# Kernel tuning notes

Hardware: AMD Instinct MI355X
Metric: run time of the kernel (lower is better)

Reference implementation:

```python
import jax, jax.numpy as jnp
import numpy as np
from jax import lax

N, CIN, FMAPS, H, W, K, LATENT = 8, 512, 512, 64, 64, 3, 512
LRMUL = 1.0
# StyleGAN2 wscale: he_std = gain/sqrt(fan_in); runtime_coef = he_std*lrmul; init_std = 1/lrmul = 1
COEF_W = 1.0 / np.sqrt(K * K * CIN)   # fan_in of conv weight
COEF_S = 1.0 / np.sqrt(LATENT)        # fan_in of modulation dense


def setup_inputs() -> dict:
    key = jax.random.key(0)
    k1, k2, k3, k4, k5 = jax.random.split(key, 5)
    return {
        "x": jax.random.normal(k1, (N, CIN, H, W), jnp.float32),
        "dlatent_vect": jax.random.normal(k2, (N, LATENT), jnp.float32),
        "weight": jax.random.normal(k3, (K, K, CIN, FMAPS), jnp.float32),
        "mod_weight": jax.random.normal(k4, (LATENT, CIN), jnp.float32),
        "mod_bias": jax.random.normal(k5, (CIN,), jnp.float32),
    }


def reference(x, dlatent_vect, weight, mod_weight, mod_bias):
    n = x.shape[0]
    w = weight * COEF_W                                   # [K,K,CIN,FMAPS]
    # style: s = dlatent @ (mod_weight*coef) + bias*lrmul + 1
    s = dlatent_vect @ (mod_weight * COEF_S) + mod_bias * LRMUL + 1.0  # [N,CIN]
    # modulate per-sample weights
    ww = w[None] * s[:, None, None, :, None]              # [N,K,K,CIN,FMAPS]
    # demodulate
    d = lax.rsqrt(jnp.sum(jnp.square(ww), axis=(1, 2, 3)) + 1e-8)  # [N,FMAPS]
    ww = ww * d[:, None, None, None, :]
    # fused modconv: batch-as-groups grouped conv
    x_g = x.reshape(1, n * CIN, H, W)
    w_g = jnp.transpose(ww, (1, 2, 3, 0, 4)).reshape(K, K, CIN, n * FMAPS)
    out = lax.conv_general_dilated(
        x_g, w_g,
        window_strides=(1, 1), padding="SAME",
        dimension_numbers=("NCHW", "HWIO", "NCHW"),
        feature_group_count=n,
    )  # [1, N*FMAPS, H, W]
    return out.reshape(n, FMAPS, H, W)
```

## Files before the change

kernel.cpp:

```cpp
#include <hip/hip_runtime.h>
#include <stdint.h>

typedef unsigned short u16;
typedef __bf16 bf16x8 __attribute__((ext_vector_type(8)));
typedef float  f32x16 __attribute__((ext_vector_type(16)));
typedef short  short8v __attribute__((ext_vector_type(8)));

#define COEF_S 0.044194173824159216f
#define COEF_W 0.014731391274719738f

static __device__ __forceinline__ bf16x8 as_b(short8v v) {
  union { short8v s; bf16x8 b; } u; u.s = v; return u.b;
}

__global__ void style_k(const float* __restrict__ dl, const float* __restrict__ mw,
                        const float* __restrict__ mb, float* __restrict__ s) {
  int idx = blockIdx.x * 256 + threadIdx.x;
  int n = idx >> 9, c = idx & 511;
  const float* dln = dl + n * 512;
  float acc = 0.f;
  for (int l = 0; l < 512; ++l) acc = fmaf(dln[l], mw[l * 512 + c], acc);
  s[idx] = acc * COEF_S + mb[c] + 1.0f;
}

__global__ void wsq_k(const float* __restrict__ w, float* __restrict__ wsq) {
  int idx = blockIdx.x * 256 + threadIdx.x;
  float acc = 0.f;
#pragma unroll
  for (int t = 0; t < 9; ++t) { float v = w[t * 262144 + idx]; acc = fmaf(v, v, acc); }
  wsq[idx] = acc * (1.0f / 4608.0f);
}

__global__ void dcoef_k(const float* __restrict__ s, const float* __restrict__ wsq,
                        float* __restrict__ d) {
  int idx = blockIdx.x * 256 + threadIdx.x;
  int n = idx >> 9, f = idx & 511;
  const float* sn = s + n * 512;
  float acc = 0.f;
  for (int c = 0; c < 512; ++c) { float sv = sn[c]; acc = fmaf(sv * sv, wsq[c * 512 + f], acc); }
  d[idx] = 1.0f / sqrtf(acc + 1e-8f);
}

__global__ void wsplit_k(const float* __restrict__ w, u16* __restrict__ whi,
                         u16* __restrict__ wlo) {
  __shared__ float T[64 * 68];
  int bid = blockIdx.x;
  int tap = bid >> 6, r = bid & 63;
  int f0 = (r >> 3) * 64, c0 = (r & 7) * 64;
  int t = threadIdx.x;
#pragma unroll
  for (int rep = 0; rep < 4; ++rep) {
    int slot = rep * 256 + t;
    int cl = slot >> 4, fq = slot & 15;
    float4 v = *(const float4*)(w + (tap * 512 + c0 + cl) * 512 + f0 + 4 * fq);
    v.x *= COEF_W; v.y *= COEF_W; v.z *= COEF_W; v.w *= COEF_W;
    *(float4*)(T + cl * 68 + 4 * fq) = v;
  }
  __syncthreads();
#pragma unroll
  for (int rep = 0; rep < 16; ++rep) {
    int slot = rep * 256 + t;
    int fl = slot >> 6, cl = slot & 63;
    float v = T[cl * 68 + fl];
    unsigned b = __float_as_uint(v);
    u16 hi = (u16)(b >> 16);
    float rem = v - __uint_as_float(b & 0xffff0000u);
    u16 lo = (u16)(__float_as_uint(rem) >> 16);
    int oidx = (tap * 512 + f0 + fl) * 512 + c0 + cl;
    whi[oidx] = hi;
    wlo[oidx] = lo;
  }
}

#define CPAD 40
__launch_bounds__(256, 2)
__global__ void conv_k(const float* __restrict__ x, const float* __restrict__ s,
                       const float* __restrict__ dco,
                       const u16* __restrict__ whi, const u16* __restrict__ wlo,
                       float* __restrict__ out) {
  __shared__ u16 Xh[6 * 66 * CPAD];
  __shared__ u16 Xl[6 * 66 * CPAD];

  int bid = blockIdx.x;
  int n = bid >> 6;
  int r = bid & 63;
  int ft = r >> 4;
  int rt = r & 15;
  int h0 = rt * 4;
  int tid = threadIdx.x;
  int lane = tid & 63;
  int wav = tid >> 6;
  int wm = wav >> 1, wn = wav & 1;
  int fw = ft * 128 + wm * 64;
  int pxw = wn * 128;
  int li = lane & 31;
  int lq = lane >> 5;

  f32x16 acc[2][4];
#pragma unroll
  for (int a = 0; a < 2; ++a)
#pragma unroll
    for (int b = 0; b < 4; ++b)
#pragma unroll
      for (int e = 0; e < 16; ++e) acc[a][b][e] = 0.0f;

  for (int slot = tid; slot < 384; slot += 256) {
    int sr = slot >> 6; int e = (slot >> 5) & 1; int cc = slot & 31;
    int off = (sr * 66 + (e ? 65 : 0)) * CPAD + cc;
    Xh[off] = 0; Xl[off] = 0;
  }

  const float* xn = x + n * 512 * 64 * 64;
  const float* sn = s + n * 512;

  for (int c0 = 0; c0 < 512; c0 += 32) {
    __syncthreads();
#pragma unroll
    for (int rep = 0; rep < 12; ++rep) {
      int slot = rep * 256 + tid;
      int row = slot >> 4;
      int q = slot & 15;
      int cc = row & 31, sr = row >> 5;
      int h = h0 - 1 + sr;
      float sv = sn[c0 + cc];
      float4 v = make_float4(0.f, 0.f, 0.f, 0.f);
      if (h >= 0 && h < 64) v = *(const float4*)(xn + ((c0 + cc) * 64 + h) * 64 + 4 * q);
      float vv[4] = {v.x * sv, v.y * sv, v.z * sv, v.w * sv};
      int ob = (sr * 66 + 1 + 4 * q) * CPAD + cc;
#pragma unroll
      for (int j = 0; j < 4; ++j) {
        unsigned b = __float_as_uint(vv[j]);
        u16 hi = (u16)(b >> 16);
        float rem = vv[j] - __uint_as_float(b & 0xffff0000u);
        u16 lo = (u16)(__float_as_uint(rem) >> 16);
        Xh[ob + j * CPAD] = hi;
        Xl[ob + j * CPAD] = lo;
      }
    }
    __syncthreads();
    for (int ky = 0; ky < 3; ++ky) {
#pragma unroll
      for (int kx = 0; kx < 3; ++kx) {
#pragma unroll
        for (int ks = 0; ks < 2; ++ks) {
          int cidx = c0 + ks * 16 + lq * 8;
          bf16x8 ah[2], al[2];
#pragma unroll
          for (int fm = 0; fm < 2; ++fm) {
            int widx = ((ky * 3 + kx) * 512 + fw + fm * 32 + li) * 512 + cidx;
            ah[fm] = as_b(*(const short8v*)(whi + widx));
            al[fm] = as_b(*(const short8v*)(wlo + widx));
          }
#pragma unroll
          for (int pn = 0; pn < 4; ++pn) {
            int srow = ((pxw + pn * 32) >> 6) + ky;
            int scol = (pn & 1) * 32 + li + kx;
            int loff = (srow * 66 + scol) * CPAD + ks * 16 + lq * 8;
            bf16x8 bh = as_b(*(const short8v*)(Xh + loff));
            bf16x8 bl = as_b(*(const short8v*)(Xl + loff));
            acc[0][pn] = __builtin_amdgcn_mfma_f32_32x32x16_bf16(ah[0], bh, acc[0][pn], 0, 0, 0);
            acc[1][pn] = __builtin_amdgcn_mfma_f32_32x32x16_bf16(ah[1], bh, acc[1][pn], 0, 0, 0);
            acc[0][pn] = __builtin_amdgcn_mfma_f32_32x32x16_bf16(ah[0], bl, acc[0][pn], 0, 0, 0);
            acc[1][pn] = __builtin_amdgcn_mfma_f32_32x32x16_bf16(ah[1], bl, acc[1][pn], 0, 0, 0);
            acc[0][pn] = __builtin_amdgcn_mfma_f32_32x32x16_bf16(al[0], bh, acc[0][pn], 0, 0, 0);
            acc[1][pn] = __builtin_amdgcn_mfma_f32_32x32x16_bf16(al[1], bh, acc[1][pn], 0, 0, 0);
          }
        }
      }
    }
  }

  const float* dn = dco + n * 512;
  float* on = out + n * 512 * 64 * 64;
#pragma unroll
  for (int fm = 0; fm < 2; ++fm) {
#pragma unroll
    for (int pn = 0; pn < 4; ++pn) {
      int px = pxw + pn * 32 + li;
      int h = h0 + (px >> 6);
      int wcol = px & 63;
#pragma unroll
      for (int e = 0; e < 16; ++e) {
        int f = fw + fm * 32 + (e & 3) + 8 * (e >> 2) + 4 * lq;
        on[(f * 64 + h) * 64 + wcol] = acc[fm][pn][e] * dn[f];
      }
    }
  }
}

extern "C" void kernel_launch(void* const* d_in, const int* in_sizes, int n_in,
                              void* d_out, int out_size, void* d_ws, size_t ws_size,
                              hipStream_t stream) {
  const float* x  = (const float*)d_in[0];
  const float* dl = (const float*)d_in[1];
  const float* w  = (const float*)d_in[2];
  const float* mw = (const float*)d_in[3];
  const float* mb = (const float*)d_in[4];
  float* out = (float*)d_out;

  char* wsb = (char*)d_ws;
  float* s_ws  = (float*)wsb;
  float* d_ws2 = (float*)(wsb + 16384);
  float* wsq_w = (float*)(wsb + 32768);
  u16*   whi   = (u16*)(wsb + 32768 + 1048576);
  u16*   wlo   = whi + 9 * 512 * 512;

  style_k<<<16, 256, 0, stream>>>(dl, mw, mb, s_ws);
  wsq_k<<<1024, 256, 0, stream>>>(w, wsq_w);
  dcoef_k<<<16, 256, 0, stream>>>(s_ws, wsq_w, d_ws2);
  wsplit_k<<<576, 256, 0, stream>>>(w, whi, wlo);
  conv_k<<<512, 256, 0, stream>>>(x, s_ws, d_ws2, whi, wlo, out);
}
```

Baseline: 554.4 us.

## Reassign wave tiles to 128 filters by 64 pixels and vectorize X staging

Each wave now covers all 128 output filters of the block and 64 pixels, where before it covered 64 filters and 128 pixels. This changes the mix of global weight loads and LDS activation reads per MFMA: every wave now loads the full 128-filter weight slice from global, and each LDS activation fragment is reused across four filter tiles. The X staging loop is also rewritten so each lane loads 8 channels for one column and writes them with a single 16-byte LDS store instead of scattered 2-byte stores. The weight global traffic per block doubles, but LDS store instructions drop and the global reads stay coalesced along the row.

```diff
diff --git a/kernel.cpp b/kernel.cpp
--- a/kernel.cpp
+++ b/kernel.cpp
@@ -90,17 +90,16 @@
   int tid = threadIdx.x;
   int lane = tid & 63;
   int wav = tid >> 6;
-  int wm = wav >> 1, wn = wav & 1;
-  int fw = ft * 128 + wm * 64;
-  int pxw = wn * 128;
+  int fw = ft * 128;
+  int pxw = wav * 64;
   int li = lane & 31;
   int lq = lane >> 5;
 
-  f32x16 acc[2][4];
-#pragma unroll
-  for (int a = 0; a < 2; ++a)
-#pragma unroll
-    for (int b = 0; b < 4; ++b)
+  f32x16 acc[4][2];
+#pragma unroll
+  for (int a = 0; a < 4; ++a)
+#pragma unroll
+    for (int b = 0; b < 2; ++b)
 #pragma unroll
       for (int e = 0; e < 16; ++e) acc[a][b][e] = 0.0f;
 
@@ -116,26 +115,28 @@
   for (int c0 = 0; c0 < 512; c0 += 32) {
     __syncthreads();
 #pragma unroll
-    for (int rep = 0; rep < 12; ++rep) {
-      int slot = rep * 256 + tid;
-      int row = slot >> 4;
-      int q = slot & 15;
-      int cc = row & 31, sr = row >> 5;
+    for (int k = 0; k < 6; ++k) {
+      int sr = k;
+      int cgrp = wav;
       int h = h0 - 1 + sr;
-      float sv = sn[c0 + cc];
-      float4 v = make_float4(0.f, 0.f, 0.f, 0.f);
-      if (h >= 0 && h < 64) v = *(const float4*)(xn + ((c0 + cc) * 64 + h) * 64 + 4 * q);
-      float vv[4] = {v.x * sv, v.y * sv, v.z * sv, v.w * sv};
-      int ob = (sr * 66 + 1 + 4 * q) * CPAD + cc;
-#pragma unroll
-      for (int j = 0; j < 4; ++j) {
-        unsigned b = __float_as_uint(vv[j]);
-        u16 hi = (u16)(b >> 16);
-        float rem = vv[j] - __uint_as_float(b & 0xffff0000u);
-        u16 lo = (u16)(__float_as_uint(rem) >> 16);
-        Xh[ob + j * CPAD] = hi;
-        Xl[ob + j * CPAD] = lo;
+      bool ok = (h >= 0) && (h < 64);
+      const float* xb = xn + (c0 + cgrp * 8) * 4096 + h * 64 + lane;
+      float v[8];
+#pragma unroll
+      for (int j = 0; j < 8; ++j) v[j] = ok ? xb[j * 4096] : 0.0f;
+      union { short8v v; u16 a[8]; } hi8, lo8;
+#pragma unroll
+      for (int j = 0; j < 8; ++j) {
+        float sv = sn[c0 + cgrp * 8 + j];
+        float t = v[j] * sv;
+        unsigned b = __float_as_uint(t);
+        hi8.a[j] = (u16)(b >> 16);
+        float rem = t - __uint_as_float(b & 0xffff0000u);
+        lo8.a[j] = (u16)(__float_as_uint(rem) >> 16);
       }
+      int ob = (sr * 66 + 1 + lane) * CPAD + cgrp * 8;
+      *(short8v*)(Xh + ob) = hi8.v;
+      *(short8v*)(Xl + ob) = lo8.v;
     }
     __syncthreads();
     for (int ky = 0; ky < 3; ++ky) {
@@ -144,26 +145,27 @@
 #pragma unroll
         for (int ks = 0; ks < 2; ++ks) {
           int cidx = c0 + ks * 16 + lq * 8;
-          bf16x8 ah[2], al[2];
-#pragma unroll
-          for (int fm = 0; fm < 2; ++fm) {
+          bf16x8 ah[4], al[4];
+#pragma unroll
+          for (int fm = 0; fm < 4; ++fm) {
             int widx = ((ky * 3 + kx) * 512 + fw + fm * 32 + li) * 512 + cidx;
             ah[fm] = as_b(*(const short8v*)(whi + widx));
             al[fm] = as_b(*(const short8v*)(wlo + widx));
           }
 #pragma unroll
-          for (int pn = 0; pn < 4; ++pn) {
-            int srow = ((pxw + pn * 32) >> 6) + ky;
-            int scol = (pn & 1) * 32 + li + kx;
+          for (int pn = 0; pn < 2; ++pn) {
+            int px0 = pxw + pn * 32;
+            int srow = (px0 >> 6) + ky;
+            int scol = (px0 & 63) + li + kx;
             int loff = (srow * 66 + scol) * CPAD + ks * 16 + lq * 8;
             bf16x8 bh = as_b(*(const short8v*)(Xh + loff));
             bf16x8 bl = as_b(*(const short8v*)(Xl + loff));
-            acc[0][pn] = __builtin_amdgcn_mfma_f32_32x32x16_bf16(ah[0], bh, acc[0][pn], 0, 0, 0);
-            acc[1][pn] = __builtin_amdgcn_mfma_f32_32x32x16_bf16(ah[1], bh, acc[1][pn], 0, 0, 0);
-            acc[0][pn] = __builtin_amdgcn_mfma_f32_32x32x16_bf16(ah[0], bl, acc[0][pn], 0, 0, 0);
-            acc[1][pn] = __builtin_amdgcn_mfma_f32_32x32x16_bf16(ah[1], bl, acc[1][pn], 0, 0, 0);
-            acc[0][pn] = __builtin_amdgcn_mfma_f32_32x32x16_bf16(al[0], bh, acc[0][pn], 0, 0, 0);
-            acc[1][pn] = __builtin_amdgcn_mfma_f32_32x32x16_bf16(al[1], bh, acc[1][pn], 0, 0, 0);
+#pragma unroll
+            for (int fm = 0; fm < 4; ++fm) {
+              acc[fm][pn] = __builtin_amdgcn_mfma_f32_32x32x16_bf16(ah[fm], bh, acc[fm][pn], 0, 0, 0);
+              acc[fm][pn] = __builtin_amdgcn_mfma_f32_32x32x16_bf16(ah[fm], bl, acc[fm][pn], 0, 0, 0);
+              acc[fm][pn] = __builtin_amdgcn_mfma_f32_32x32x16_bf16(al[fm], bh, acc[fm][pn], 0, 0, 0);
+            }
           }
         }
       }
@@ -173,9 +175,9 @@
   const float* dn = dco + n * 512;
   float* on = out + n * 512 * 64 * 64;
 #pragma unroll
-  for (int fm = 0; fm < 2; ++fm) {
-#pragma unroll
-    for (int pn = 0; pn < 4; ++pn) {
+  for (int fm = 0; fm < 4; ++fm) {
+#pragma unroll
+    for (int pn = 0; pn < 2; ++pn) {
       int px = pxw + pn * 32 + li;
       int h = h0 + (px >> 6);
       int wcol = px & 63;
```

After: 724.1 us. 1.31x slower.
